# Kernel tuning notes

Hardware: AMD Instinct MI355X
Metric: run time of the kernel (lower is better)

The kernel has to match this reference:

```python
import jax, jax.numpy as jnp
import numpy as np

# Structure constants (equal-sized graphs; first SPG nodes of each graph are sentence nodes)
B = 64          # graphs in batch
NPG = 1024      # nodes per graph
SPG = 64        # sentence nodes per graph
N = B * NPG     # 65536 total nodes
E = 524288      # total edges (within-graph)
C = 256         # in_channels
H = 512         # TopKPooling hardcoded hidden
KS = 3          # num_output_sentences
KO = int(np.ceil(0.5 * (NPG - SPG)))  # ratio=0.5 -> 480 'other' nodes kept per graph
SLOPE = 0.01    # LeakyReLU default negative slope


def gcn_conv(x, row, col, w, W, b, n):
    """PyG GCNConv with edge_weight: add self-loops (weight 1), symmetric norm, aggregate at col."""
    loop = jnp.arange(n, dtype=row.dtype)
    row2 = jnp.concatenate([row, loop])
    col2 = jnp.concatenate([col, loop])
    w2 = jnp.concatenate([w, jnp.ones((n,), w.dtype)])
    deg = jax.ops.segment_sum(w2, col2, num_segments=n)
    dinv = jnp.where(deg > 0, jax.lax.rsqrt(jnp.where(deg > 0, deg, 1.0)), 0.0)
    norm = dinv[row2] * w2 * dinv[col2]          # [E+N]
    h = x @ W                                     # [N, out]
    out = jax.ops.segment_sum(norm[:, None] * h[row2], col2, num_segments=n)
    return out + b


def setup_inputs() -> dict:
    key = jax.random.key(0)
    ks = jax.random.split(key, 6)
    x = jax.random.normal(ks[0], (N, C), jnp.float32)
    # within-graph random edges
    gid = jnp.arange(E, dtype=jnp.int32) // (E // B)
    src = jax.random.randint(ks[1], (E,), 0, NPG, dtype=jnp.int32) + gid * NPG
    dst = jax.random.randint(ks[2], (E,), 0, NPG, dtype=jnp.int32) + gid * NPG
    edge_index = jnp.stack([src, dst], axis=0)
    edge_attr = jax.random.uniform(ks[3], (E, 1), jnp.float32, 0.1, 1.0)
    batch = jnp.repeat(jnp.arange(B, dtype=jnp.int32), NPG)
    W1 = jax.random.normal(ks[4], (C, H), jnp.float32) * (1.0 / np.sqrt(C))
    b1 = jnp.zeros((H,), jnp.float32)
    W2 = jax.random.normal(ks[5], (H, 1), jnp.float32) * (1.0 / np.sqrt(H))
    b2 = jnp.zeros((1,), jnp.float32)
    return {"x": x, "edge_index": edge_index, "edge_attr": edge_attr, "batch": batch,
            "W1": W1, "b1": b1, "W2": W2, "b2": b2}


def reference(x, edge_index, edge_attr, batch, W1, b1, W2, b2):
    row, col = edge_index[0], edge_index[1]
    w = edge_attr[:, 0]                           # edge_weight = edge_attr.squeeze()
    # 2-layer GCN scorer
    h = gcn_conv(x, row, col, w, W1, b1, N)
    h = jnp.where(h > 0, h, SLOPE * h)            # LeakyReLU
    score = gcn_conv(h, row, col, w, W2, b2, N)[:, 0]
    score = jnp.nan_to_num(score)
    sg = score.reshape(B, NPG)                    # dense per-graph scores (graphs equal-sized)
    # per-graph top-k: 3 sentence nodes, ceil(0.5*other) other nodes
    _, si = jax.lax.top_k(sg[:, :SPG], KS)        # [B, KS] local idx among sentence nodes
    sent_perm = (si + jnp.arange(B)[:, None] * NPG).reshape(-1)
    _, oi = jax.lax.top_k(sg[:, SPG:], KO)        # [B, KO] local idx among other nodes
    other_perm = (oi + SPG + jnp.arange(B)[:, None] * NPG).reshape(-1)
    perm = jnp.concatenate([sent_perm, other_perm])  # [B*(KS+KO)]
    # gather + scale (multiplier = 1)
    score_perm = score[perm]
    x_out = x[perm] * score_perm[:, None]
    batch_out = batch[perm]
    # filter_adj (padded: dropped edges marked -1 / zeroed; 'keep' mask returned)
    mask = jnp.full((N,), -1, dtype=perm.dtype).at[perm].set(jnp.arange(perm.shape[0], dtype=perm.dtype))
    nr, nc = mask[row], mask[col]
    keep = (nr >= 0) & (nc >= 0)
    ei_new = jnp.where(keep, jnp.stack([nr, nc], axis=0), -1)
    ea_new = jnp.where(keep[:, None], edge_attr, 0.0)
    sentence_scores = sg[:, :SPG].reshape(-1)
    sentence_batch = jnp.repeat(jnp.arange(B, dtype=batch.dtype), SPG)
    return (x_out, ei_new, ea_new, batch_out, perm, score_perm, sentence_scores, sentence_batch, keep)
```

## Files before the change

### kernel.cpp

```cpp
#include <hip/hip_runtime.h>

#define NN   65536
#define NE   524288
#define EPG  8192

#define O1 7913472
#define O2 8962048
#define O3 9486336
#define O4 9517248
#define O5 9548160
#define O6 9579072
#define O7 9583168
#define O8 9587264

#define CSR_OFF    8388608
#define DINV_OFF   9437184
#define Z_OFF      9502720
#define W1HI_OFF   9568256
#define RSTART_OFF 9633792
#define CURSOR_OFF 9699344
#define W1LO_OFF   9764880
#define HIST_OFF   9830416
#define YLO_OFF    4194304

typedef __attribute__((ext_vector_type(8))) short bfrag;
typedef __attribute__((ext_vector_type(4))) float f32x4;
typedef __attribute__((ext_vector_type(8))) unsigned short us8;
typedef __attribute__((ext_vector_type(2))) unsigned long long u64x2;

__device__ __forceinline__ unsigned monof(float f) {
  unsigned u = __float_as_uint(f);
  return (u & 0x80000000u) ? ~u : (u | 0x80000000u);
}

__device__ __forceinline__ unsigned short bf16rne(float f) {
  unsigned u = __float_as_uint(f);
  return (unsigned short)((u + 0x7FFFu + ((u >> 16) & 1u)) >> 16);
}

__global__ __launch_bounds__(256) void k_zero_w1t(unsigned long long* __restrict__ hist,
    float* __restrict__ z, const float* __restrict__ W1,
    unsigned short* __restrict__ hi, unsigned short* __restrict__ lo) {
  __shared__ unsigned short sh[64][72], sl[64][72];
  int b = blockIdx.x, t = threadIdx.x;
  if (b < 256) {
    int n = b * 256 + t;
    hist[n] = 0ull;
    z[n] = 0.0f;
    return;
  }
  int bb = b - 256;
  int bk = bb & 3, bc = bb >> 2;
  int k0 = bk * 64, c0 = bc * 64;
#pragma unroll
  for (int s = 0; s < 16; ++s) {
    int i = t + s * 256;
    int k = i >> 6, c = i & 63;
    float v = W1[(k0 + k) * 512 + c0 + c];
    unsigned short h = bf16rne(v);
    float hf = __uint_as_float((unsigned)h << 16);
    sh[c][k] = h;
    sl[c][k] = bf16rne(v - hf);
  }
  __syncthreads();
#pragma unroll
  for (int s = 0; s < 16; ++s) {
    int i = t + s * 256;
    int c = i >> 6, k = i & 63;
    hi[(c0 + c) * 256 + k0 + k] = sh[c][k];
    lo[(c0 + c) * 256 + k0 + k] = sl[c][k];
  }
}

__global__ void k_hist(const int* __restrict__ ei, const float* __restrict__ w,
                       unsigned long long* __restrict__ hist) {
  int e = blockIdx.x * 256 + threadIdx.x;
  if (e < NE) {
    int c = ei[NE + e];
    unsigned long long add = (1ull << 40) |
        (unsigned long long)(unsigned)__float2uint_rn(w[e] * 1048576.0f);
    atomicAdd(&hist[c], add);
  }
}

__global__ __launch_bounds__(256) void k_prefix(const unsigned long long* __restrict__ hist,
    unsigned* __restrict__ rstart, unsigned* __restrict__ cursor, float* __restrict__ dinv) {
  __shared__ unsigned tmp[2][256];
  int g = blockIdx.x, t = threadIdx.x;
  int base = g << 10;
  unsigned c[4], sum = 0;
  unsigned long long hv[4];
#pragma unroll
  for (int u = 0; u < 4; ++u) {
    hv[u] = hist[base + t * 4 + u];
    c[u] = (unsigned)(hv[u] >> 40);
    sum += c[u];
  }
  tmp[0][t] = sum;
  __syncthreads();
  int pin = 0;
  for (int off = 1; off < 256; off <<= 1) {
    int pout = pin ^ 1;
    unsigned v = tmp[pin][t];
    if (t >= off) v += tmp[pin][t - off];
    tmp[pout][t] = v;
    __syncthreads();
    pin = pout;
  }
  unsigned run = (t == 0) ? 0u : tmp[pin][t - 1];
#pragma unroll
  for (int u = 0; u < 4; ++u) {
    unsigned pos = (unsigned)(g << 13) + run;
    rstart[base + t * 4 + u] = pos;
    cursor[base + t * 4 + u] = pos;
    run += c[u];
  }
#pragma unroll
  for (int u = 0; u < 4; ++u) {
    int n = base + t * 4 + u;
    float wsum = 1.0f + (float)(hv[u] & ((1ull << 40) - 1)) * 9.5367431640625e-07f;
    dinv[n] = rsqrtf(wsum);
  }
  if (g == 0 && t == 0) rstart[NN] = NE;
}

__global__ void k_scatter(const int* __restrict__ ei, const float* __restrict__ w,
                          const float* __restrict__ dinv, unsigned* __restrict__ cursor,
                          unsigned long long* __restrict__ csr) {
  int e = blockIdx.x * 256 + threadIdx.x;
  if (e < NE) {
    int r = ei[e], c = ei[NE + e];
    float cf = w[e] * dinv[r] * dinv[c];
    unsigned pos = atomicAdd(&cursor[c], 1u);
    unsigned sl = (unsigned)(r & 1023);
    csr[pos] = ((unsigned long long)__float_as_uint(cf) << 32) |
               (sl << 15) | (sl * 17u);
  }
}

__global__ __launch_bounds__(1024, 1) void k_aggx(const float* __restrict__ x,
    const unsigned long long* __restrict__ csr, const unsigned* __restrict__ rstart,
    const float* __restrict__ dinv, unsigned short* __restrict__ yhi,
    unsigned short* __restrict__ ylo, int gbase) {
  __shared__ float xs[1024 * 17];
  __shared__ unsigned long long es[8193];
  __shared__ unsigned rp[1025];
  __shared__ float dv2[1024];
  int bid = blockIdx.x;
  int g  = bid & 31;
  int cc = bid >> 5;
  int gg = gbase + g;
  int c0 = cc * 16;
  int t = threadIdx.x;
  int nbase = gg << 10;
  unsigned ebase = (unsigned)gg << 13;
  {
    rp[t] = rstart[nbase + t] - ebase;
    float dv = dinv[nbase + t];
    dv2[t] = dv * dv;
  }
  if (t == 0) { rp[1024] = 8192u; es[8192] = 0ull; }
  {
    const u64x2* src = (const u64x2*)(csr + ebase);
    u64x2* dst = (u64x2*)es;
#pragma unroll
    for (int i = 0; i < 4; ++i)
      dst[t + i * 1024] = src[t + i * 1024];
  }
#pragma unroll
  for (int s = 0; s < 4; ++s) {
    int i = t + s * 1024;
    int row = i >> 2, q = (i & 3) * 4;
    float4 v = *(const float4*)&x[(nbase + row) * 256 + c0 + q];
    float* d = &xs[row * 17 + q];
    d[0] = v.x; d[1] = v.y; d[2] = v.z; d[3] = v.w;
  }
  __syncthreads();
  int jj = t & 7;
  int h  = (t >> 3) & 1;
  int grp = t >> 4;
  int dbase = grp * 16;
  int j2 = 2 * jj;
  for (int dd = 0; dd < 8; ++dd) {
    int d0 = dbase + dd;
    unsigned pA = rp[d0], qA = rp[d0 + 1];
    unsigned pB = rp[d0 + 8], qB = rp[d0 + 9];
    int L0 = (int)(qA - pA), L1 = (int)(qB - pB);
    int L = L0 > L1 ? L0 : L1;
    int d = d0 + 8 * h;
    unsigned p = h ? pB : pA;
    unsigned q = h ? qB : qA;
    int dofs = d * 17 + j2;
    float dv = dv2[d];
    float ax = dv * xs[dofs], ay = dv * xs[dofs + 1];
    for (int k = 0; k < L; k += 4) {
      unsigned long long cv[4];
#pragma unroll
      for (int u = 0; u < 4; ++u) {
        unsigned a = p + (unsigned)(k + u);
        cv[u] = es[a < q ? a : 8192u];
      }
#pragma unroll
      for (int u = 0; u < 4; ++u) {
        float cf = __uint_as_float((unsigned)(cv[u] >> 32));
        unsigned o = ((unsigned)cv[u] & 0x7FFFu) + (unsigned)j2;
        ax += cf * xs[o];
        ay += cf * xs[o + 1];
      }
    }
    int idx = ((g << 10) + d) * 256 + c0 + j2;
    unsigned short hx = bf16rne(ax), hy = bf16rne(ay);
    float lx = ax - __uint_as_float((unsigned)hx << 16);
    float ly = ay - __uint_as_float((unsigned)hy << 16);
    *(unsigned*)&yhi[idx] = (unsigned)hx | ((unsigned)hy << 16);
    *(unsigned*)&ylo[idx] = (unsigned)bf16rne(lx) | ((unsigned)bf16rne(ly) << 16);
  }
}

__global__ __launch_bounds__(256, 3) void k_gemm(
    const unsigned short* __restrict__ yhi, const unsigned short* __restrict__ ylo,
    const unsigned short* __restrict__ w1hi, const unsigned short* __restrict__ w1lo,
    const float* __restrict__ b1, const float* __restrict__ W2,
    float* __restrict__ z, int node_base) {
  __shared__ unsigned short Ah_s[128 * 40], Al_s[128 * 40];
  __shared__ unsigned short Bh_s[128 * 40], Bl_s[128 * 40];
  int bx = blockIdx.x & 3, by = blockIdx.x >> 2;
  int r0 = by * 128, c0 = bx * 128;
  int t = threadIdx.x;
  int lane = t & 63, wid = t >> 6;
  int wr = wid >> 1, wc = wid & 1;
  int lr = lane & 15, hg = lane >> 4;
  f32x4 acc[4][4];
#pragma unroll
  for (int m = 0; m < 4; ++m)
#pragma unroll
    for (int n = 0; n < 4; ++n)
      acc[m][n] = (f32x4){0.0f, 0.0f, 0.0f, 0.0f};
  int rr = t >> 2, kq = (t & 3) * 8;
  for (int kt = 0; kt < 256; kt += 32) {
    us8 va0 = *(const us8*)&yhi[(r0 + rr) * 256 + kt + kq];
    us8 va1 = *(const us8*)&yhi[(r0 + rr + 64) * 256 + kt + kq];
    us8 vb0 = *(const us8*)&ylo[(r0 + rr) * 256 + kt + kq];
    us8 vb1 = *(const us8*)&ylo[(r0 + rr + 64) * 256 + kt + kq];
    us8 vc0 = *(const us8*)&w1hi[(c0 + rr) * 256 + kt + kq];
    us8 vc1 = *(const us8*)&w1hi[(c0 + rr + 64) * 256 + kt + kq];
    us8 vd0 = *(const us8*)&w1lo[(c0 + rr) * 256 + kt + kq];
    us8 vd1 = *(const us8*)&w1lo[(c0 + rr + 64) * 256 + kt + kq];
    __syncthreads();
    *(us8*)&Ah_s[rr * 40 + kq] = va0;  *(us8*)&Ah_s[(rr + 64) * 40 + kq] = va1;
    *(us8*)&Al_s[rr * 40 + kq] = vb0;  *(us8*)&Al_s[(rr + 64) * 40 + kq] = vb1;
    *(us8*)&Bh_s[rr * 40 + kq] = vc0;  *(us8*)&Bh_s[(rr + 64) * 40 + kq] = vc1;
    *(us8*)&Bl_s[rr * 40 + kq] = vd0;  *(us8*)&Bl_s[(rr + 64) * 40 + kq] = vd1;
    __syncthreads();
    bfrag Ah[4], Al[4], Bh[4], Bl[4];
#pragma unroll
    for (int m = 0; m < 4; ++m) {
      int ra = (wr * 64 + m * 16 + lr) * 40 + hg * 8;
      Ah[m] = *(const bfrag*)&Ah_s[ra];
      Al[m] = *(const bfrag*)&Al_s[ra];
      int rb = (wc * 64 + m * 16 + lr) * 40 + hg * 8;
      Bh[m] = *(const bfrag*)&Bh_s[rb];
      Bl[m] = *(const bfrag*)&Bl_s[rb];
    }
#pragma unroll
    for (int m = 0; m < 4; ++m)
#pragma unroll
      for (int n = 0; n < 4; ++n) {
        acc[m][n] = __builtin_amdgcn_mfma_f32_16x16x32_bf16(Ah[m], Bh[n], acc[m][n], 0, 0, 0);
        acc[m][n] = __builtin_amdgcn_mfma_f32_16x16x32_bf16(Ah[m], Bl[n], acc[m][n], 0, 0, 0);
        acc[m][n] = __builtin_amdgcn_mfma_f32_16x16x32_bf16(Al[m], Bh[n], acc[m][n], 0, 0, 0);
      }
  }
  float p[4][4];
#pragma unroll
  for (int m = 0; m < 4; ++m)
#pragma unroll
    for (int i = 0; i < 4; ++i) p[m][i] = 0.0f;
#pragma unroll
  for (int n = 0; n < 4; ++n) {
    int col = c0 + wc * 64 + n * 16 + lr;
    float b1v = b1[col], w2v = W2[col];
#pragma unroll
    for (int m = 0; m < 4; ++m)
#pragma unroll
      for (int i = 0; i < 4; ++i) {
        float v = acc[m][n][i] + b1v;
        v = v > 0.0f ? v : 0.01f * v;
        p[m][i] += v * w2v;
      }
  }
#pragma unroll
  for (int off = 8; off > 0; off >>= 1)
#pragma unroll
    for (int m = 0; m < 4; ++m)
#pragma unroll
      for (int i = 0; i < 4; ++i)
        p[m][i] += __shfl_xor(p[m][i], off, 16);
  if (lr == 0) {
    int rbase = node_base + r0 + wr * 64 + hg * 4;
#pragma unroll
    for (int m = 0; m < 4; ++m)
#pragma unroll
      for (int i = 0; i < 4; ++i)
        unsafeAtomicAdd(&z[rbase + m * 16 + i], p[m][i]);
  }
}

__device__ void bitonic(unsigned long long* keys, int n, int t, int nt) {
  for (int k = 2; k <= n; k <<= 1)
    for (int jj = k >> 1; jj > 0; jj >>= 1) {
      __syncthreads();
      for (int i = t; i < n; i += nt) {
        int ixj = i ^ jj;
        if (ixj > i) {
          unsigned long long a = keys[i], c = keys[ixj];
          bool up = ((i & k) == 0);
          if ((a > c) == up) { keys[i] = c; keys[ixj] = a; }
        }
      }
    }
  __syncthreads();
}

__global__ __launch_bounds__(1024) void k_score_topk(
    const unsigned long long* __restrict__ csr, const unsigned* __restrict__ rstart,
    const float* __restrict__ dinv, const float* __restrict__ z,
    const float* __restrict__ b2, int* __restrict__ mask, float* __restrict__ out) {
  __shared__ float sc[1024];
  __shared__ unsigned long long keys[1024];
  int b = blockIdx.x, t = threadIdx.x;
  int base = b << 10;
  int n = base + t;
  mask[n] = -1;
  float dv = dinv[n];
  float a = b2[0] + dv * dv * z[n];
  unsigned s = rstart[n], epos = rstart[n + 1];
  for (unsigned e = s; e < epos; ++e) {
    unsigned long long p = csr[e];
    a += __uint_as_float((unsigned)(p >> 32)) * z[base + (((unsigned)p >> 15) & 1023u)];
  }
  sc[t] = a;
  if (t < 64) {
    out[O6 + b * 64 + t] = a;
    out[O7 + b * 64 + t] = (float)b;
    keys[t] = ((unsigned long long)(~monof(a)) << 32) | (unsigned)t;
  }
  __syncthreads();
  bitonic(keys, 64, t, 1024);
  if (t < 3) {
    int idx = (int)(keys[t] & 0xFFFFFFFFull);
    int node = base + idx;
    int pos = b * 3 + t;
    mask[node] = pos;
    out[O4 + pos] = (float)node;
    out[O5 + pos] = sc[idx];
    out[O3 + pos] = (float)b;
  }
  __syncthreads();
  keys[t] = (t < 960)
      ? (((unsigned long long)(~monof(sc[64 + t])) << 32) | (unsigned)t)
      : 0xFFFFFFFFFFFFFFFFull;
  __syncthreads();
  bitonic(keys, 1024, t, 1024);
  if (t < 480) {
    int idx = (int)(keys[t] & 0xFFFFFFFFull);
    int node = base + 64 + idx;
    int pos = 192 + b * 480 + t;
    mask[node] = pos;
    out[O4 + pos] = (float)node;
    out[O5 + pos] = sc[64 + idx];
    out[O3 + pos] = (float)b;
  }
}

__global__ __launch_bounds__(256) void k_tail(const int* __restrict__ ei,
    const float* __restrict__ w, const int* __restrict__ mask,
    const float* __restrict__ x, float* __restrict__ out) {
  int bid = blockIdx.x, t = threadIdx.x;
  if (bid < 2048) {
    int e = bid * 256 + t;
    int nr = mask[ei[e]];
    int nc = mask[ei[NE + e]];
    bool keep = (nr >= 0) && (nc >= 0);
    out[O1 + e]      = keep ? (float)nr : -1.0f;
    out[O1 + NE + e] = keep ? (float)nc : -1.0f;
    out[O2 + e]      = keep ? w[e] : 0.0f;
    out[O8 + e]      = keep ? 1.0f : 0.0f;
  } else {
    int i = (bid - 2048) * 4 + (t >> 6);
    int lane = t & 63;
    int node = (int)out[O4 + i];
    float s = out[O5 + i];
    float4 v = ((const float4*)&x[node * 256])[lane];
    ((float4*)&out[i * 256])[lane] = make_float4(v.x * s, v.y * s, v.z * s, v.w * s);
  }
}

extern "C" void kernel_launch(void* const* d_in, const int* in_sizes, int n_in,
                              void* d_out, int out_size, void* d_ws, size_t ws_size,
                              hipStream_t stream) {
  (void)in_sizes; (void)n_in; (void)out_size; (void)d_ws; (void)ws_size;
  const float* x  = (const float*)d_in[0];
  const int*   ei = (const int*)d_in[1];
  const float* w  = (const float*)d_in[2];
  const float* W1 = (const float*)d_in[4];
  const float* b1 = (const float*)d_in[5];
  const float* W2 = (const float*)d_in[6];
  const float* b2 = (const float*)d_in[7];
  float* out    = (float*)d_out;
  unsigned short* yhi = (unsigned short*)out;
  unsigned short* ylo = (unsigned short*)(out + YLO_OFF);
  unsigned long long* csr = (unsigned long long*)(out + CSR_OFF);
  float* dinv   = out + DINV_OFF;
  float* z      = out + Z_OFF;
  unsigned* rstart = (unsigned*)(out + RSTART_OFF);
  unsigned* cursor = (unsigned*)(out + CURSOR_OFF);
  unsigned long long* hist64 = (unsigned long long*)(out + HIST_OFF);
  unsigned short* w1hi = (unsigned short*)(out + W1HI_OFF);
  unsigned short* w1lo = (unsigned short*)(out + W1LO_OFF);
  int*   mask   = (int*)d_out;

  k_zero_w1t<<<288, 256, 0, stream>>>(hist64, z, W1, w1hi, w1lo);
  k_hist<<<2048, 256, 0, stream>>>(ei, w, hist64);
  k_prefix<<<64, 256, 0, stream>>>(hist64, rstart, cursor, dinv);
  k_scatter<<<2048, 256, 0, stream>>>(ei, w, dinv, cursor, csr);
  for (int ch = 0; ch < 2; ++ch) {
    k_aggx<<<512, 1024, 0, stream>>>(x, csr, rstart, dinv, yhi, ylo, ch * 32);
    k_gemm<<<1024, 256, 0, stream>>>(yhi, ylo, w1hi, w1lo, b1, W2, z, ch * 32768);
  }
  k_score_topk<<<64, 1024, 0, stream>>>(csr, rstart, dinv, z, b2, mask, out);
  k_tail<<<2048 + 7728, 256, 0, stream>>>(ei, w, mask, x, out);
}
```

Measured before the change: 225.5 us.

## Widen GEMM tile to 128x256 with 512 threads and register-prefetch next K slice

The GEMM block now covers 128 rows by 256 columns using 8 waves, so each A tile loaded from global memory is reused across twice as many output columns and the grid halves. Global loads for the next K slice are issued right after the shared-memory barrier, so they overlap with the MFMA work on the current slice. This trades more LDS per block and lower occupancy (2 blocks per CU of 512 threads) for less A-operand traffic and hidden load latency. The epilogue that reduces through W2 must still handle the changed wave layout (wc now 0-3).

```diff
diff --git a/kernel.cpp b/kernel.cpp
--- a/kernel.cpp
+++ b/kernel.cpp
@@ -217,18 +217,18 @@
   }
 }
 
-__global__ __launch_bounds__(256, 3) void k_gemm(
+__global__ __launch_bounds__(512, 2) void k_gemm(
     const unsigned short* __restrict__ yhi, const unsigned short* __restrict__ ylo,
     const unsigned short* __restrict__ w1hi, const unsigned short* __restrict__ w1lo,
     const float* __restrict__ b1, const float* __restrict__ W2,
     float* __restrict__ z, int node_base) {
   __shared__ unsigned short Ah_s[128 * 40], Al_s[128 * 40];
-  __shared__ unsigned short Bh_s[128 * 40], Bl_s[128 * 40];
-  int bx = blockIdx.x & 3, by = blockIdx.x >> 2;
-  int r0 = by * 128, c0 = bx * 128;
+  __shared__ unsigned short Bh_s[256 * 40], Bl_s[256 * 40];
+  int bx = blockIdx.x & 1, by = blockIdx.x >> 1;
+  int r0 = by * 128, c0 = bx * 256;
   int t = threadIdx.x;
   int lane = t & 63, wid = t >> 6;
-  int wr = wid >> 1, wc = wid & 1;
+  int wr = wid >> 2, wc = wid & 3;
   int lr = lane & 15, hg = lane >> 4;
   f32x4 acc[4][4];
 #pragma unroll
@@ -236,22 +236,31 @@
 #pragma unroll
     for (int n = 0; n < 4; ++n)
       acc[m][n] = (f32x4){0.0f, 0.0f, 0.0f, 0.0f};
-  int rr = t >> 2, kq = (t & 3) * 8;
+  int ar = t >> 2, ak = (t & 3) * 8;
+  int bc = t >> 1, bk = (t & 1) * 16;
+  us8 va, vb, vc0, vc1, vd0, vd1;
+  va  = *(const us8*)&yhi [(r0 + ar) * 256 + ak];
+  vb  = *(const us8*)&ylo [(r0 + ar) * 256 + ak];
+  vc0 = *(const us8*)&w1hi[(c0 + bc) * 256 + bk];
+  vc1 = *(const us8*)&w1hi[(c0 + bc) * 256 + bk + 8];
+  vd0 = *(const us8*)&w1lo[(c0 + bc) * 256 + bk];
+  vd1 = *(const us8*)&w1lo[(c0 + bc) * 256 + bk + 8];
   for (int kt = 0; kt < 256; kt += 32) {
-    us8 va0 = *(const us8*)&yhi[(r0 + rr) * 256 + kt + kq];
-    us8 va1 = *(const us8*)&yhi[(r0 + rr + 64) * 256 + kt + kq];
-    us8 vb0 = *(const us8*)&ylo[(r0 + rr) * 256 + kt + kq];
-    us8 vb1 = *(const us8*)&ylo[(r0 + rr + 64) * 256 + kt + kq];
-    us8 vc0 = *(const us8*)&w1hi[(c0 + rr) * 256 + kt + kq];
-    us8 vc1 = *(const us8*)&w1hi[(c0 + rr + 64) * 256 + kt + kq];
-    us8 vd0 = *(const us8*)&w1lo[(c0 + rr) * 256 + kt + kq];
-    us8 vd1 = *(const us8*)&w1lo[(c0 + rr + 64) * 256 + kt + kq];
     __syncthreads();
-    *(us8*)&Ah_s[rr * 40 + kq] = va0;  *(us8*)&Ah_s[(rr + 64) * 40 + kq] = va1;
-    *(us8*)&Al_s[rr * 40 + kq] = vb0;  *(us8*)&Al_s[(rr + 64) * 40 + kq] = vb1;
-    *(us8*)&Bh_s[rr * 40 + kq] = vc0;  *(us8*)&Bh_s[(rr + 64) * 40 + kq] = vc1;
-    *(us8*)&Bl_s[rr * 40 + kq] = vd0;  *(us8*)&Bl_s[(rr + 64) * 40 + kq] = vd1;
+    *(us8*)&Ah_s[ar * 40 + ak] = va;
+    *(us8*)&Al_s[ar * 40 + ak] = vb;
+    *(us8*)&Bh_s[bc * 40 + bk] = vc0;
+    *(us8*)&Bh_s[bc * 40 + bk + 8] = vc1;
+    *(us8*)&Bl_s[bc * 40 + bk] = vd0;
+    *(us8*)&Bl_s[bc * 40 + bk + 8] = vd1;
     __syncthreads();
+    int kn = (kt + 32 < 256) ? kt + 32 : kt;
+    va  = *(const us8*)&yhi [(r0 + ar) * 256 + kn + ak];
+    vb  = *(const us8*)&ylo [(r0 + ar) * 256 + kn + ak];
+    vc0 = *(const us8*)&w1hi[(c0 + bc) * 256 + kn + bk];
+    vc1 = *(const us8*)&w1hi[(c0 + bc) * 256 + kn + bk + 8];
+    vd0 = *(const us8*)&w1lo[(c0 + bc) * 256 + kn + bk];
+    vd1 = *(const us8*)&w1lo[(c0 + bc) * 256 + kn + bk + 8];
     bfrag Ah[4], Al[4], Bh[4], Bl[4];
 #pragma unroll
     for (int m = 0; m < 4; ++m) {
@@ -426,7 +435,7 @@
   k_scatter<<<2048, 256, 0, stream>>>(ei, w, dinv, cursor, csr);
   for (int ch = 0; ch < 2; ++ch) {
     k_aggx<<<512, 1024, 0, stream>>>(x, csr, rstart, dinv, yhi, ylo, ch * 32);
-    k_gemm<<<1024, 256, 0, stream>>>(yhi, ylo, w1hi, w1lo, b1, W2, z, ch * 32768);
+    k_gemm<<<512, 512, 0, stream>>>(yhi, ylo, w1hi, w1lo, b1, W2, z, ch * 32768);
   }
   k_score_topk<<<64, 1024, 0, stream>>>(csr, rstart, dinv, z, b2, mask, out);
   k_tail<<<2048 + 7728, 256, 0, stream>>>(ei, w, mask, x, out);
```

New measurement: 222.5 us. Within noise of the previous version (-1.4%).
